# Kernel tuning notes

Measured on AMD Instinct MI355X. Metric: run time of the kernel, lower is better.

Reference implementation:

```python
import jax, jax.numpy as jnp
import numpy as np

B, N_IN, N_OUT, K, V = 8, 2048, 2048, 64, 64


def setup_inputs() -> dict:
    key = jax.random.key(0)
    k1, k2, k3 = jax.random.split(key, 3)
    return {
        "key": jax.random.normal(k1, (B, N_IN, 1, K), dtype=jnp.float32),
        "query": jax.random.normal(k2, (B, 1, N_OUT, K), dtype=jnp.float32),
        "value": jax.random.normal(k3, (B, N_IN, V), dtype=jnp.float32),
    }


def reference(key, query, value):
    ks = key.shape[-1]
    # sum(key * query, 3) / sqrt(key_size)  ==  batched GEMM over key_size
    # weights: [B, n_inputs, n_outputs]
    weights = jnp.einsum("bik,bok->bio", key[:, :, 0, :], query[:, 0, :, :]) / jnp.sqrt(
        jnp.asarray(ks, dtype=key.dtype)
    )
    weights = jax.nn.softmax(weights, axis=1)  # softmax over n_inputs
    # sum(weights[...,None] * value[:,:,None,:], 1) -> [B, n_outputs, value_size]
    vals = jnp.einsum("bio,biv->bov", weights, value)
    # row-wise L2 normalize each [value_size] vector
    vals = vals / (jnp.linalg.norm(vals, axis=-1, keepdims=True) + 1e-12)
    values = jnp.swapaxes(vals, 1, 2)  # [B, value_size, n_outputs]
    return values, weights
```

## Files before the change

### kernel.cpp

```cpp
#include <hip/hip_runtime.h>

#define NB 8
#define NN 2048
#define KK 64
#define VV 64
#define SCALE 0.18033688011112043f

typedef __bf16 bfrag __attribute__((ext_vector_type(8)));
typedef float f32x4 __attribute__((ext_vector_type(4)));
typedef unsigned short u16x4 __attribute__((ext_vector_type(4)));
typedef unsigned short u16x8 __attribute__((ext_vector_type(8)));

__device__ __forceinline__ unsigned short bf16r(float f) {
  unsigned u = __float_as_uint(f);
  u += 0x7fffu + ((u >> 16) & 1u);
  return (unsigned short)(u >> 16);
}

__device__ __forceinline__ int swz(int row, int colByte) {
  return row * 128 + (colByte ^ ((row & 7) << 4));
}

__device__ __forceinline__ bfrag lds_frag(const unsigned short* base, int row, int colByte) {
  return *reinterpret_cast<const bfrag*>(reinterpret_cast<const char*>(base) + swz(row, colByte));
}

__device__ __forceinline__ bfrag g_frag(const float* __restrict__ g) {
  const float4* p = reinterpret_cast<const float4*>(g);
  float4 x = p[0], y = p[1];
  u16x8 u;
  u[0] = bf16r(x.x); u[1] = bf16r(x.y); u[2] = bf16r(x.z); u[3] = bf16r(x.w);
  u[4] = bf16r(y.x); u[5] = bf16r(y.y); u[6] = bf16r(y.z); u[7] = bf16r(y.w);
  union { u16x8 a; bfrag b; } c; c.a = u; return c.b;
}

struct KS { float4 f[4]; };
__device__ __forceinline__ void k_load(KS& s, const float* __restrict__ g) {
  const float4* p = reinterpret_cast<const float4*>(g);
  s.f[0] = p[0]; s.f[1] = p[1]; s.f[2] = p[2]; s.f[3] = p[3];
}
__device__ __forceinline__ void k_write(const KS& s, unsigned short* lds, int row, int colByte) {
  const float* f = reinterpret_cast<const float*>(&s.f[0]);
  u16x8 a, b;
#pragma unroll
  for (int j = 0; j < 8; ++j) a[j] = bf16r(f[j]);
#pragma unroll
  for (int j = 0; j < 8; ++j) b[j] = bf16r(f[8 + j]);
  *reinterpret_cast<u16x8*>(reinterpret_cast<char*>(lds) + swz(row, colByte)) = a;
  *reinterpret_cast<u16x8*>(reinterpret_cast<char*>(lds) + swz(row, colByte + 16)) = b;
}

struct VS { float4 f[4]; };
__device__ __forceinline__ void v_load(VS& s, const float* __restrict__ g) {
  const float4* p = reinterpret_cast<const float4*>(g);
  s.f[0] = p[0]; s.f[1] = p[1];
  const float4* q = reinterpret_cast<const float4*>(g + VV);
  s.f[2] = q[0]; s.f[3] = q[1];
}
__device__ __forceinline__ void v_write(const VS& s, unsigned short* lds, int il, int v0) {
  const float* lo = reinterpret_cast<const float*>(&s.f[0]);
  const float* hi = reinterpret_cast<const float*>(&s.f[2]);
#pragma unroll
  for (int j = 0; j < 8; ++j) {
    unsigned pk = (unsigned)bf16r(lo[j]) | ((unsigned)bf16r(hi[j]) << 16);
    *reinterpret_cast<unsigned*>(reinterpret_cast<char*>(lds) + swz(v0 + j, il * 2)) = pk;
  }
}

#define CHUNK 512
#define IT 64
#define K1STEPS (CHUNK / IT)
#define SCR_STRIDE 4160

__global__ void __launch_bounds__(256) attn_pass1(
    const float* __restrict__ key, const float* __restrict__ query,
    const float* __restrict__ value, float* __restrict__ scratch)
{
  __shared__ __align__(16) unsigned short Kt[IT * KK];
  __shared__ __align__(16) unsigned short Vt[VV * IT];
  __shared__ __align__(16) unsigned short Et[64 * IT];
  __shared__ float Red[4][64];

  const int tid  = threadIdx.x;
  const int lane = tid & 63;
  const int wv   = tid >> 6;
  const int l15  = lane & 15;
  const int l4   = lane >> 4;

  const int b    = blockIdx.x & 7;
  const int rest = blockIdx.x >> 3;
  const int ot   = rest & 31;
  const int ci   = rest >> 5;
  const int o0   = ot * 64;
  const int ib0  = ci * CHUNK;

  const float* Kg = key   + (size_t)b * NN * KK;
  const float* Qg = query + (size_t)b * NN * KK;
  const float* Vg = value + (size_t)b * NN * VV;
  float* scr = scratch + (size_t)((b * 32 + ot) * 4 + ci) * SCR_STRIDE;

  const int krow = tid >> 2;
  const int kel  = (tid & 3) * 16;
  const int kcb  = (tid & 3) * 32;
  const int vil  = (tid & 31) * 2;
  const int vv0  = (tid >> 5) * 8;

  bfrag qb0[4], qb1[4];
#pragma unroll
  for (int s = 0; s < 4; ++s) {
    const float* qr = Qg + (size_t)(o0 + s * 16 + l15) * KK;
    qb0[s] = g_frag(qr + l4 * 8);
    qb1[s] = g_frag(qr + 32 + l4 * 8);
  }

  KS ks; VS vs;
  k_load(ks, Kg + (size_t)(ib0 + krow) * KK + kel);
  v_load(vs, Vg + (size_t)(ib0 + vil) * VV + vv0);
  k_write(ks, Kt, krow, kcb);
  v_write(vs, Vt, vil, vv0);
  __syncthreads();

  f32x4 uacc[4];
  float Dacc[4] = {0.f, 0.f, 0.f, 0.f};
#pragma unroll
  for (int s = 0; s < 4; ++s) { f32x4 z = {0.f, 0.f, 0.f, 0.f}; uacc[s] = z; }

  for (int t = 0; t < K1STEPS; ++t) {
    if (t + 1 < K1STEPS) {
      k_load(ks, Kg + (size_t)(ib0 + (t + 1) * IT + krow) * KK + kel);
      v_load(vs, Vg + (size_t)(ib0 + (t + 1) * IT + vil) * VV + vv0);
    }
    bfrag a0 = lds_frag(Kt, wv * 16 + l15, l4 * 16);
    bfrag a1 = lds_frag(Kt, wv * 16 + l15, 64 + l4 * 16);
#pragma unroll
    for (int s = 0; s < 4; ++s) {
      f32x4 z = {0.f, 0.f, 0.f, 0.f};
      z = __builtin_amdgcn_mfma_f32_16x16x32_bf16(a0, qb0[s], z, 0, 0, 0);
      z = __builtin_amdgcn_mfma_f32_16x16x32_bf16(a1, qb1[s], z, 0, 0, 0);
      f32x4 e;
#pragma unroll
      for (int r = 0; r < 4; ++r) e[r] = exp2f(z[r] * SCALE);
      Dacc[s] += e[0] + e[1] + e[2] + e[3];
      u16x4 pk;
#pragma unroll
      for (int r = 0; r < 4; ++r) pk[r] = bf16r(e[r]);
      *reinterpret_cast<u16x4*>(reinterpret_cast<char*>(Et) +
                                swz(s * 16 + l15, wv * 32 + l4 * 8)) = pk;
    }
    __syncthreads();
    if (t + 1 < K1STEPS) k_write(ks, Kt, krow, kcb);
    bfrag va0 = lds_frag(Vt, wv * 16 + l15, l4 * 16);
    bfrag va1 = lds_frag(Vt, wv * 16 + l15, 64 + l4 * 16);
#pragma unroll
    for (int s = 0; s < 4; ++s) {
      bfrag e0 = lds_frag(Et, s * 16 + l15, l4 * 16);
      bfrag e1 = lds_frag(Et, s * 16 + l15, 64 + l4 * 16);
      uacc[s] = __builtin_amdgcn_mfma_f32_16x16x32_bf16(va0, e0, uacc[s], 0, 0, 0);
      uacc[s] = __builtin_amdgcn_mfma_f32_16x16x32_bf16(va1, e1, uacc[s], 0, 0, 0);
    }
    __syncthreads();
    if (t + 1 < K1STEPS) v_write(vs, Vt, vil, vv0);
  }

#pragma unroll
  for (int s = 0; s < 4; ++s)
#pragma unroll
    for (int r = 0; r < 4; ++r)
      scr[(wv * 16 + l4 * 4 + r) * 64 + s * 16 + l15] = uacc[s][r];

#pragma unroll
  for (int s = 0; s < 4; ++s) {
    float d = Dacc[s];
    d += __shfl_xor(d, 16, 64);
    d += __shfl_xor(d, 32, 64);
    if (lane < 16) Red[wv][s * 16 + lane] = d;
  }
  __syncthreads();
  if (tid < 64)
    scr[4096 + tid] = Red[0][tid] + Red[1][tid] + Red[2][tid] + Red[3][tid];
}

__global__ void __launch_bounds__(512) attn_reduce(
    const float* __restrict__ scratch, float* __restrict__ outV,
    float* __restrict__ invD)
{
  __shared__ float R2[8][64];
  __shared__ float Nn[64];

  const int tid = threadIdx.x;
  const int b   = blockIdx.x & 7;
  const int ot  = blockIdx.x >> 3;
  const float* base = scratch + (size_t)(b * 32 + ot) * 4 * SCR_STRIDE;

  const int ol = tid & 63;
  const int vg = tid >> 6;

  float u[8];
#pragma unroll
  for (int j = 0; j < 8; ++j) u[j] = 0.f;
#pragma unroll
  for (int c = 0; c < 4; ++c) {
    const float* p = base + c * SCR_STRIDE;
#pragma unroll
    for (int j = 0; j < 8; ++j) u[j] += p[(vg + 8 * j) * 64 + ol];
  }
  float ssq = 0.f;
#pragma unroll
  for (int j = 0; j < 8; ++j) ssq += u[j] * u[j];
  R2[vg][ol] = ssq;
  __syncthreads();
  if (tid < 64) {
    float n = 0.f;
#pragma unroll
    for (int g = 0; g < 8; ++g) n += R2[g][tid];
    Nn[tid] = 1.f / (sqrtf(n) + 1e-12f);
    float D = 0.f;
#pragma unroll
    for (int c = 0; c < 4; ++c) D += base[c * SCR_STRIDE + 4096 + tid];
    invD[b * NN + ot * 64 + tid] = 1.f / D;
  }
  __syncthreads();
  const float inn = Nn[ol];
  float* vp = outV + (size_t)b * VV * NN + ot * 64 + ol;
#pragma unroll
  for (int j = 0; j < 8; ++j)
    vp[(size_t)(vg + 8 * j) * NN] = u[j] * inn;
}

__global__ void __launch_bounds__(256) attn_weights(
    const float* __restrict__ key, const float* __restrict__ query,
    const float* __restrict__ invD, float* __restrict__ outWall)
{
  __shared__ __align__(16) unsigned short Kt2[128 * 64];

  const int tid  = threadIdx.x;
  const int lane = tid & 63;
  const int wv   = tid >> 6;
  const int l15  = lane & 15;
  const int l4   = lane >> 4;

  const int b    = blockIdx.x & 7;
  const int rest = blockIdx.x >> 3;
  const int it   = rest & 15;
  const int ot   = rest >> 4;

  const float* Kg = key   + (size_t)b * NN * KK;
  const float* Qg = query + (size_t)b * NN * KK;
  float* outW = outWall + (size_t)b * NN * NN;

  {
    const int krow = tid >> 1;
    const int half = (tid & 1);
    KS sA, sB;
    k_load(sA, Kg + (size_t)(it * 128 + krow) * KK + half * 32);
    k_load(sB, Kg + (size_t)(it * 128 + krow) * KK + half * 32 + 16);
    k_write(sA, Kt2, krow, half * 64);
    k_write(sB, Kt2, krow, half * 64 + 32);
  }

  bfrag a0[2], a1[2];
#pragma unroll
  for (int m = 0; m < 2; ++m) {
    const float* qr = Qg + (size_t)(ot * 128 + wv * 32 + m * 16 + l15) * KK;
    a0[m] = g_frag(qr + l4 * 8);
    a1[m] = g_frag(qr + 32 + l4 * 8);
  }
  f32x4 id[2];
#pragma unroll
  for (int m = 0; m < 2; ++m)
    id[m] = *reinterpret_cast<const f32x4*>(
        &invD[b * NN + ot * 128 + wv * 32 + m * 16 + l4 * 4]);
  __syncthreads();

#pragma unroll
  for (int s = 0; s < 8; ++s) {
    bfrag b0 = lds_frag(Kt2, s * 16 + l15, l4 * 16);
    bfrag b1 = lds_frag(Kt2, s * 16 + l15, 64 + l4 * 16);
#pragma unroll
    for (int m = 0; m < 2; ++m) {
      f32x4 z = {0.f, 0.f, 0.f, 0.f};
      z = __builtin_amdgcn_mfma_f32_16x16x32_bf16(a0[m], b0, z, 0, 0, 0);
      z = __builtin_amdgcn_mfma_f32_16x16x32_bf16(a1[m], b1, z, 0, 0, 0);
      f32x4 w;
#pragma unroll
      for (int r = 0; r < 4; ++r) w[r] = exp2f(z[r] * SCALE) * id[m][r];
      float* wp = outW + (size_t)(it * 128 + s * 16 + l15) * NN +
                  ot * 128 + wv * 32 + m * 16 + l4 * 4;
      *reinterpret_cast<f32x4*>(wp) = w;
    }
  }
}

extern "C" void kernel_launch(void* const* d_in, const int* in_sizes, int n_in,
                              void* d_out, int out_size, void* d_ws, size_t ws_size,
                              hipStream_t stream) {
  (void)in_sizes; (void)n_in; (void)ws_size; (void)out_size;
  const float* key   = (const float*)d_in[0];
  const float* query = (const float*)d_in[1];
  const float* value = (const float*)d_in[2];
  float* out  = (float*)d_out;
  float* outV = out;
  float* outW = out + (size_t)NB * VV * NN;
  float* invD = (float*)d_ws;
  float* scratch = outW;

  attn_pass1 <<<dim3(NB * 32 * 4), dim3(256), 0, stream>>>(key, query, value, scratch);
  attn_reduce<<<dim3(NB * 32),     dim3(512), 0, stream>>>(scratch, outV, invD);
  attn_weights<<<dim3(NB * 16 * 16), dim3(256), 0, stream>>>(key, query, invD, outW);
}
```

Before: 76.35 us.

## Restructure attention into denom pass, fused weights+PV main pass, and normalize pass

```diff
diff --git a/kernel.cpp b/kernel.cpp
--- a/kernel.cpp
+++ b/kernel.cpp
@@ -6,48 +6,26 @@
 #define VV 64
 #define SCALE 0.18033688011112043f
 
-typedef __bf16 bfrag __attribute__((ext_vector_type(8)));
-typedef float f32x4 __attribute__((ext_vector_type(4)));
-typedef unsigned short u16x4 __attribute__((ext_vector_type(4)));
-typedef unsigned short u16x8 __attribute__((ext_vector_type(8)));
-
-__device__ __forceinline__ unsigned short bf16r(float f) {
-  unsigned u = __float_as_uint(f);
-  u += 0x7fffu + ((u >> 16) & 1u);
-  return (unsigned short)(u >> 16);
-}
-
-__device__ __forceinline__ int swz(int row, int colByte) {
-  return row * 128 + (colByte ^ ((row & 7) << 4));
+typedef __bf16 bfrag  __attribute__((ext_vector_type(8)));
+typedef __bf16 bf16x4 __attribute__((ext_vector_type(4)));
+typedef float  f32x4  __attribute__((ext_vector_type(4)));
+
+__device__ __forceinline__ int swz256(int row, int colByte) {
+  return row * 256 + (colByte ^ ((row & 7) << 4));
 }
 
 __device__ __forceinline__ bfrag lds_frag(const unsigned short* base, int row, int colByte) {
-  return *reinterpret_cast<const bfrag*>(reinterpret_cast<const char*>(base) + swz(row, colByte));
+  return *reinterpret_cast<const bfrag*>(
+      reinterpret_cast<const char*>(base) + swz256(row, colByte));
 }
 
 __device__ __forceinline__ bfrag g_frag(const float* __restrict__ g) {
   const float4* p = reinterpret_cast<const float4*>(g);
   float4 x = p[0], y = p[1];
-  u16x8 u;
-  u[0] = bf16r(x.x); u[1] = bf16r(x.y); u[2] = bf16r(x.z); u[3] = bf16r(x.w);
-  u[4] = bf16r(y.x); u[5] = bf16r(y.y); u[6] = bf16r(y.z); u[7] = bf16r(y.w);
-  union { u16x8 a; bfrag b; } c; c.a = u; return c.b;
-}
-
-struct KS { float4 f[4]; };
-__device__ __forceinline__ void k_load(KS& s, const float* __restrict__ g) {
-  const float4* p = reinterpret_cast<const float4*>(g);
-  s.f[0] = p[0]; s.f[1] = p[1]; s.f[2] = p[2]; s.f[3] = p[3];
-}
-__device__ __forceinline__ void k_write(const KS& s, unsigned short* lds, int row, int colByte) {
-  const float* f = reinterpret_cast<const float*>(&s.f[0]);
-  u16x8 a, b;
-#pragma unroll
-  for (int j = 0; j < 8; ++j) a[j] = bf16r(f[j]);
-#pragma unroll
-  for (int j = 0; j < 8; ++j) b[j] = bf16r(f[8 + j]);
-  *reinterpret_cast<u16x8*>(reinterpret_cast<char*>(lds) + swz(row, colByte)) = a;
-  *reinterpret_cast<u16x8*>(reinterpret_cast<char*>(lds) + swz(row, colByte + 16)) = b;
+  bfrag r;
+  r[0] = (__bf16)x.x; r[1] = (__bf16)x.y; r[2] = (__bf16)x.z; r[3] = (__bf16)x.w;
+  r[4] = (__bf16)y.x; r[5] = (__bf16)y.y; r[6] = (__bf16)y.z; r[7] = (__bf16)y.w;
+  return r;
 }
 
 struct VS { float4 f[4]; };
@@ -62,23 +40,16 @@
   const float* hi = reinterpret_cast<const float*>(&s.f[2]);
 #pragma unroll
   for (int j = 0; j < 8; ++j) {
-    unsigned pk = (unsigned)bf16r(lo[j]) | ((unsigned)bf16r(hi[j]) << 16);
-    *reinterpret_cast<unsigned*>(reinterpret_cast<char*>(lds) + swz(v0 + j, il * 2)) = pk;
-  }
-}
-
-#define CHUNK 512
-#define IT 64
-#define K1STEPS (CHUNK / IT)
-#define SCR_STRIDE 4160
-
-__global__ void __launch_bounds__(256) attn_pass1(
+    __bf16 two[2] = { (__bf16)lo[j], (__bf16)hi[j] };
+    *reinterpret_cast<unsigned*>(reinterpret_cast<char*>(lds) + swz256(v0 + j, il * 2)) =
+        *reinterpret_cast<unsigned*>(two);
+  }
+}
+
+__global__ void __launch_bounds__(256) attn_denom(
     const float* __restrict__ key, const float* __restrict__ query,
-    const float* __restrict__ value, float* __restrict__ scratch)
+    float* __restrict__ dpart, float* __restrict__ uzero)
 {
-  __shared__ __align__(16) unsigned short Kt[IT * KK];
-  __shared__ __align__(16) unsigned short Vt[VV * IT];
-  __shared__ __align__(16) unsigned short Et[64 * IT];
   __shared__ float Red[4][64];
 
   const int tid  = threadIdx.x;
@@ -91,82 +62,38 @@
   const int rest = blockIdx.x >> 3;
   const int ot   = rest & 31;
   const int ci   = rest >> 5;
-  const int o0   = ot * 64;
-  const int ib0  = ci * CHUNK;
 
   const float* Kg = key   + (size_t)b * NN * KK;
   const float* Qg = query + (size_t)b * NN * KK;
-  const float* Vg = value + (size_t)b * NN * VV;
-  float* scr = scratch + (size_t)((b * 32 + ot) * 4 + ci) * SCR_STRIDE;
-
-  const int krow = tid >> 2;
-  const int kel  = (tid & 3) * 16;
-  const int kcb  = (tid & 3) * 32;
-  const int vil  = (tid & 31) * 2;
-  const int vv0  = (tid >> 5) * 8;
-
-  bfrag qb0[4], qb1[4];
+
+  {
+    float4 z4 = {0.f, 0.f, 0.f, 0.f};
+    reinterpret_cast<float4*>(uzero)[(size_t)blockIdx.x * 256 + tid] = z4;
+  }
+
+  bfrag qb[4][2];
 #pragma unroll
   for (int s = 0; s < 4; ++s) {
-    const float* qr = Qg + (size_t)(o0 + s * 16 + l15) * KK;
-    qb0[s] = g_frag(qr + l4 * 8);
-    qb1[s] = g_frag(qr + 32 + l4 * 8);
-  }
-
-  KS ks; VS vs;
-  k_load(ks, Kg + (size_t)(ib0 + krow) * KK + kel);
-  v_load(vs, Vg + (size_t)(ib0 + vil) * VV + vv0);
-  k_write(ks, Kt, krow, kcb);
-  v_write(vs, Vt, vil, vv0);
-  __syncthreads();
-
-  f32x4 uacc[4];
+    const float* qr = Qg + (size_t)(ot * 64 + s * 16 + l15) * KK;
+    qb[s][0] = g_frag(qr + l4 * 8);
+    qb[s][1] = g_frag(qr + 32 + l4 * 8);
+  }
+
   float Dacc[4] = {0.f, 0.f, 0.f, 0.f};
-#pragma unroll
-  for (int s = 0; s < 4; ++s) { f32x4 z = {0.f, 0.f, 0.f, 0.f}; uacc[s] = z; }
-
-  for (int t = 0; t < K1STEPS; ++t) {
-    if (t + 1 < K1STEPS) {
-      k_load(ks, Kg + (size_t)(ib0 + (t + 1) * IT + krow) * KK + kel);
-      v_load(vs, Vg + (size_t)(ib0 + (t + 1) * IT + vil) * VV + vv0);
-    }
-    bfrag a0 = lds_frag(Kt, wv * 16 + l15, l4 * 16);
-    bfrag a1 = lds_frag(Kt, wv * 16 + l15, 64 + l4 * 16);
+  const int ib0 = ci * 512;
+  for (int t = 0; t < 8; ++t) {
+    const float* kr = Kg + (size_t)(ib0 + t * 64 + wv * 16 + l15) * KK;
+    bfrag a0 = g_frag(kr + l4 * 8);
+    bfrag a1 = g_frag(kr + 32 + l4 * 8);
 #pragma unroll
     for (int s = 0; s < 4; ++s) {
       f32x4 z = {0.f, 0.f, 0.f, 0.f};
-      z = __builtin_amdgcn_mfma_f32_16x16x32_bf16(a0, qb0[s], z, 0, 0, 0);
-      z = __builtin_amdgcn_mfma_f32_16x16x32_bf16(a1, qb1[s], z, 0, 0, 0);
-      f32x4 e;
-#pragma unroll
-      for (int r = 0; r < 4; ++r) e[r] = exp2f(z[r] * SCALE);
-      Dacc[s] += e[0] + e[1] + e[2] + e[3];
-      u16x4 pk;
-#pragma unroll
-      for (int r = 0; r < 4; ++r) pk[r] = bf16r(e[r]);
-      *reinterpret_cast<u16x4*>(reinterpret_cast<char*>(Et) +
-                                swz(s * 16 + l15, wv * 32 + l4 * 8)) = pk;
+      z = __builtin_amdgcn_mfma_f32_16x16x32_bf16(a0, qb[s][0], z, 0, 0, 0);
+      z = __builtin_amdgcn_mfma_f32_16x16x32_bf16(a1, qb[s][1], z, 0, 0, 0);
+      Dacc[s] += exp2f(z[0] * SCALE) + exp2f(z[1] * SCALE) +
+                 exp2f(z[2] * SCALE) + exp2f(z[3] * SCALE);
     }
-    __syncthreads();
-    if (t + 1 < K1STEPS) k_write(ks, Kt, krow, kcb);
-    bfrag va0 = lds_frag(Vt, wv * 16 + l15, l4 * 16);
-    bfrag va1 = lds_frag(Vt, wv * 16 + l15, 64 + l4 * 16);
-#pragma unroll
-    for (int s = 0; s < 4; ++s) {
-      bfrag e0 = lds_frag(Et, s * 16 + l15, l4 * 16);
-      bfrag e1 = lds_frag(Et, s * 16 + l15, 64 + l4 * 16);
-      uacc[s] = __builtin_amdgcn_mfma_f32_16x16x32_bf16(va0, e0, uacc[s], 0, 0, 0);
-      uacc[s] = __builtin_amdgcn_mfma_f32_16x16x32_bf16(va1, e1, uacc[s], 0, 0, 0);
-    }
-    __syncthreads();
-    if (t + 1 < K1STEPS) v_write(vs, Vt, vil, vv0);
-  }
-
-#pragma unroll
-  for (int s = 0; s < 4; ++s)
-#pragma unroll
-    for (int r = 0; r < 4; ++r)
-      scr[(wv * 16 + l4 * 4 + r) * 64 + s * 16 + l15] = uacc[s][r];
+  }
 
 #pragma unroll
   for (int s = 0; s < 4; ++s) {
@@ -177,61 +104,18 @@
   }
   __syncthreads();
   if (tid < 64)
-    scr[4096 + tid] = Red[0][tid] + Red[1][tid] + Red[2][tid] + Red[3][tid];
-}
-
-__global__ void __launch_bounds__(512) attn_reduce(
-    const float* __restrict__ scratch, float* __restrict__ outV,
-    float* __restrict__ invD)
+    dpart[(size_t)((b * 32 + ot) * 4 + ci) * 64 + tid] =
+        Red[0][tid] + Red[1][tid] + Red[2][tid] + Red[3][tid];
+}
+
+__global__ void __launch_bounds__(256) attn_main(
+    const float* __restrict__ key, const float* __restrict__ query,
+    const float* __restrict__ value, const float* __restrict__ dpart,
+    float* __restrict__ U, float* __restrict__ Wout)
 {
-  __shared__ float R2[8][64];
-  __shared__ float Nn[64];
-
-  const int tid = threadIdx.x;
-  const int b   = blockIdx.x & 7;
-  const int ot  = blockIdx.x >> 3;
-  const float* base = scratch + (size_t)(b * 32 + ot) * 4 * SCR_STRIDE;
-
-  const int ol = tid & 63;
-  const int vg = tid >> 6;
-
-  float u[8];
-#pragma unroll
-  for (int j = 0; j < 8; ++j) u[j] = 0.f;
-#pragma unroll
-  for (int c = 0; c < 4; ++c) {
-    const float* p = base + c * SCR_STRIDE;
-#pragma unroll
-    for (int j = 0; j < 8; ++j) u[j] += p[(vg + 8 * j) * 64 + ol];
-  }
-  float ssq = 0.f;
-#pragma unroll
-  for (int j = 0; j < 8; ++j) ssq += u[j] * u[j];
-  R2[vg][ol] = ssq;
-  __syncthreads();
-  if (tid < 64) {
-    float n = 0.f;
-#pragma unroll
-    for (int g = 0; g < 8; ++g) n += R2[g][tid];
-    Nn[tid] = 1.f / (sqrtf(n) + 1e-12f);
-    float D = 0.f;
-#pragma unroll
-    for (int c = 0; c < 4; ++c) D += base[c * SCR_STRIDE + 4096 + tid];
-    invD[b * NN + ot * 64 + tid] = 1.f / D;
-  }
-  __syncthreads();
-  const float inn = Nn[ol];
-  float* vp = outV + (size_t)b * VV * NN + ot * 64 + ol;
-#pragma unroll
-  for (int j = 0; j < 8; ++j)
-    vp[(size_t)(vg + 8 * j) * NN] = u[j] * inn;
-}
-
-__global__ void __launch_bounds__(256) attn_weights(
-    const float* __restrict__ key, const float* __restrict__ query,
-    const float* __restrict__ invD, float* __restrict__ outWall)
-{
-  __shared__ __align__(16) unsigned short Kt2[128 * 64];
+  __shared__ __align__(16) unsigned short Vt[64 * 128];
+  __shared__ __align__(16) unsigned short Et[128 * 128];
+  __shared__ float InvD[128];
 
   const int tid  = threadIdx.x;
   const int lane = tid & 63;
@@ -246,48 +130,122 @@
 
   const float* Kg = key   + (size_t)b * NN * KK;
   const float* Qg = query + (size_t)b * NN * KK;
-  float* outW = outWall + (size_t)b * NN * NN;
-
-  {
-    const int krow = tid >> 1;
-    const int half = (tid & 1);
-    KS sA, sB;
-    k_load(sA, Kg + (size_t)(it * 128 + krow) * KK + half * 32);
-    k_load(sB, Kg + (size_t)(it * 128 + krow) * KK + half * 32 + 16);
-    k_write(sA, Kt2, krow, half * 64);
-    k_write(sB, Kt2, krow, half * 64 + 32);
-  }
-
-  bfrag a0[2], a1[2];
+  const float* Vg = value + (size_t)b * NN * VV;
+  float* outW = Wout + (size_t)b * NN * NN;
+
+  const int vil = (tid & 63) * 2;
+  const int vv0 = (tid >> 6) * 8;
+  VS vs0, vs1;
+  v_load(vs0, Vg + (size_t)(it * 128 + vil) * VV + vv0);
+  v_load(vs1, Vg + (size_t)(it * 128 + vil) * VV + vv0 + 32);
+
+  if (tid < 128) {
+    const int otile = ot * 2 + (tid >> 6);
+    const float* dp = dpart + (size_t)((b * 32 + otile) * 4) * 64 + (tid & 63);
+    InvD[tid] = 1.f / (dp[0] + dp[64] + dp[128] + dp[192]);
+  }
+  __syncthreads();
+  float invd[8];
+#pragma unroll
+  for (int s = 0; s < 8; ++s) invd[s] = InvD[s * 16 + l15];
+
+  bfrag aK[2][2], qb[8][2];
 #pragma unroll
   for (int m = 0; m < 2; ++m) {
-    const float* qr = Qg + (size_t)(ot * 128 + wv * 32 + m * 16 + l15) * KK;
-    a0[m] = g_frag(qr + l4 * 8);
-    a1[m] = g_frag(qr + 32 + l4 * 8);
-  }
-  f32x4 id[2];
-#pragma unroll
-  for (int m = 0; m < 2; ++m)
-    id[m] = *reinterpret_cast<const f32x4*>(
-        &invD[b * NN + ot * 128 + wv * 32 + m * 16 + l4 * 4]);
-  __syncthreads();
-
+    const float* kr = Kg + (size_t)(it * 128 + wv * 32 + m * 16 + l15) * KK;
+    aK[m][0] = g_frag(kr + l4 * 8);
+    aK[m][1] = g_frag(kr + 32 + l4 * 8);
+  }
 #pragma unroll
   for (int s = 0; s < 8; ++s) {
-    bfrag b0 = lds_frag(Kt2, s * 16 + l15, l4 * 16);
-    bfrag b1 = lds_frag(Kt2, s * 16 + l15, 64 + l4 * 16);
-#pragma unroll
-    for (int m = 0; m < 2; ++m) {
+    const float* qr = Qg + (size_t)(ot * 128 + s * 16 + l15) * KK;
+    qb[s][0] = g_frag(qr + l4 * 8);
+    qb[s][1] = g_frag(qr + 32 + l4 * 8);
+  }
+
+#pragma unroll
+  for (int m = 0; m < 2; ++m) {
+#pragma unroll
+    for (int s = 0; s < 8; ++s) {
       f32x4 z = {0.f, 0.f, 0.f, 0.f};
-      z = __builtin_amdgcn_mfma_f32_16x16x32_bf16(a0[m], b0, z, 0, 0, 0);
-      z = __builtin_amdgcn_mfma_f32_16x16x32_bf16(a1[m], b1, z, 0, 0, 0);
-      f32x4 w;
-#pragma unroll
-      for (int r = 0; r < 4; ++r) w[r] = exp2f(z[r] * SCALE) * id[m][r];
-      float* wp = outW + (size_t)(it * 128 + s * 16 + l15) * NN +
-                  ot * 128 + wv * 32 + m * 16 + l4 * 4;
-      *reinterpret_cast<f32x4*>(wp) = w;
+      z = __builtin_amdgcn_mfma_f32_16x16x32_bf16(aK[m][0], qb[s][0], z, 0, 0, 0);
+      z = __builtin_amdgcn_mfma_f32_16x16x32_bf16(aK[m][1], qb[s][1], z, 0, 0, 0);
+      f32x4 e;
+#pragma unroll
+      for (int r = 0; r < 4; ++r) e[r] = exp2f(z[r] * SCALE);
+      float* wp = outW + (size_t)(it * 128 + wv * 32 + m * 16 + l4 * 4) * NN +
+                  ot * 128 + s * 16 + l15;
+      const float iv = invd[s];
+#pragma unroll
+      for (int r = 0; r < 4; ++r) wp[(size_t)r * NN] = e[r] * iv;
+      bf16x4 pk;
+#pragma unroll
+      for (int r = 0; r < 4; ++r) pk[r] = (__bf16)e[r];
+      *reinterpret_cast<bf16x4*>(reinterpret_cast<char*>(Et) +
+          swz256(s * 16 + l15, (wv * 32 + m * 16 + l4 * 4) * 2)) = pk;
     }
+  }
+  v_write(vs0, Vt, vil, vv0);
+  v_write(vs1, Vt, vil, vv0 + 32);
+  __syncthreads();
+
+  bfrag va[4];
+#pragma unroll
+  for (int kh = 0; kh < 4; ++kh)
+    va[kh] = lds_frag(Vt, wv * 16 + l15, kh * 64 + l4 * 16);
+#pragma unroll
+  for (int s = 0; s < 8; ++s) {
+    f32x4 z = {0.f, 0.f, 0.f, 0.f};
+#pragma unroll
+    for (int kh = 0; kh < 4; ++kh) {
+      bfrag eb = lds_frag(Et, s * 16 + l15, kh * 64 + l4 * 16);
+      z = __builtin_amdgcn_mfma_f32_16x16x32_bf16(va[kh], eb, z, 0, 0, 0);
+    }
+    float* up = U + (size_t)b * VV * NN + (size_t)(wv * 16 + l4 * 4) * NN +
+                ot * 128 + s * 16 + l15;
+#pragma unroll
+    for (int r = 0; r < 4; ++r)
+      unsafeAtomicAdd(up + (size_t)r * NN, z[r]);
+  }
+}
+
+__global__ void __launch_bounds__(256) attn_norm(float* __restrict__ out)
+{
+  __shared__ float Ut[64][65];
+  __shared__ float Sc[64];
+
+  const int tid = threadIdx.x;
+  const int b   = blockIdx.x & 7;
+  const int oc  = blockIdx.x >> 3;
+  float* base = out + (size_t)b * VV * NN + oc * 64;
+
+  const int v  = tid >> 2;
+  const int oq = (tid & 3) * 16;
+
+  float x[16];
+#pragma unroll
+  for (int j = 0; j < 4; ++j) {
+    float4 f = *reinterpret_cast<const float4*>(base + (size_t)v * NN + oq + j * 4);
+    x[j * 4 + 0] = f.x; x[j * 4 + 1] = f.y; x[j * 4 + 2] = f.z; x[j * 4 + 3] = f.w;
+  }
+#pragma unroll
+  for (int k = 0; k < 16; ++k) Ut[v][oq + k] = x[k];
+  __syncthreads();
+  if (tid < 64) {
+    float ssq = 0.f;
+#pragma unroll
+    for (int vv = 0; vv < 64; ++vv) ssq += Ut[vv][tid] * Ut[vv][tid];
+    Sc[tid] = 1.f / (sqrtf(ssq) + 1e-12f);
+  }
+  __syncthreads();
+#pragma unroll
+  for (int j = 0; j < 4; ++j) {
+    float4 f;
+    f.x = x[j * 4 + 0] * Sc[oq + j * 4 + 0];
+    f.y = x[j * 4 + 1] * Sc[oq + j * 4 + 1];
+    f.z = x[j * 4 + 2] * Sc[oq + j * 4 + 2];
+    f.w = x[j * 4 + 3] * Sc[oq + j * 4 + 3];
+    *reinterpret_cast<float4*>(base + (size_t)v * NN + oq + j * 4) = f;
   }
 }
 
@@ -298,13 +256,12 @@
   const float* key   = (const float*)d_in[0];
   const float* query = (const float*)d_in[1];
   const float* value = (const float*)d_in[2];
-  float* out  = (float*)d_out;
-  float* outV = out;
-  float* outW = out + (size_t)NB * VV * NN;
-  float* invD = (float*)d_ws;
-  float* scratch = outW;
-
-  attn_pass1 <<<dim3(NB * 32 * 4), dim3(256), 0, stream>>>(key, query, value, scratch);
-  attn_reduce<<<dim3(NB * 32),     dim3(512), 0, stream>>>(scratch, outV, invD);
-  attn_weights<<<dim3(NB * 16 * 16), dim3(256), 0, stream>>>(key, query, invD, outW);
-}
+  float* out   = (float*)d_out;
+  float* U     = out;
+  float* Wgt   = out + (size_t)NB * VV * NN;
+  float* dpart = (float*)d_ws;
+
+  attn_denom<<<dim3(NB * 32 * 4), dim3(256), 0, stream>>>(key, query, dpart, U);
+  attn_main <<<dim3(NB * 16 * 16), dim3(256), 0, stream>>>(key, query, value, dpart, U, Wgt);
+  attn_norm <<<dim3(NB * 32),      dim3(256), 0, stream>>>(out);
+}
```

New measurement: 122.5 us. +60.4%, slower.
